# Kernel tuning notes

Hardware: AMD Instinct MI355X
Metric: run time of the kernel (lower is better)

The kernel has to match this reference:

```python
import jax, jax.numpy as jnp
import numpy as np

B_, L_, D_, E_, N_, DT_, K_ = 2, 1024, 1024, 2048, 16, 64, 4
EPS = 1e-5


def setup_inputs() -> dict:
    key = jax.random.key(0)
    ks = jax.random.split(key, 16)
    s = lambda *sh: 1.0 / np.sqrt(sh[-1])
    return {
        "resid": jax.random.normal(ks[0], (B_, L_, D_), jnp.float32),
        "norm_w": jnp.ones((D_,), jnp.float32),
        "skip_w": jax.random.normal(ks[1], (E_, D_), jnp.float32) * s(E_, D_),
        "in_w": jax.random.normal(ks[2], (E_, D_), jnp.float32) * s(E_, D_),
        "conv_w": jax.random.normal(ks[3], (E_, K_), jnp.float32) * s(E_, K_),
        "conv_b": jax.random.normal(ks[4], (E_,), jnp.float32) * 0.1,
        "wd1": jax.random.normal(ks[5], (DT_, E_), jnp.float32) * s(DT_, E_),
        "wd2": jax.random.normal(ks[6], (E_, DT_), jnp.float32) * s(E_, DT_),
        "wd2_b": jax.random.normal(ks[7], (E_,), jnp.float32) * 0.1,
        "wb": jax.random.normal(ks[8], (N_, E_), jnp.float32) * s(N_, E_),
        "wc": jax.random.normal(ks[9], (N_, E_), jnp.float32) * s(N_, E_),
        "A_log": jnp.log(jax.random.uniform(ks[10], (E_, N_), jnp.float32, 0.5, 4.0)),
        "W_D": jnp.ones((E_,), jnp.float32),
        "out_w": jax.random.normal(ks[11], (D_, E_), jnp.float32) * s(D_, E_),
    }


def _forward(resid, norm_w, skip_w, in_w, conv_w, conv_b, wd1, wd2, wd2_b,
             wb, wc, A_log, W_D, out_w):
    B, L, D = resid.shape
    E, N = A_log.shape
    K = conv_w.shape[-1]
    # RMSNorm
    xn = resid * jax.lax.rsqrt(jnp.mean(resid * resid, -1, keepdims=True) + EPS) * norm_w
    skip = jnp.einsum('bld,ed->ble', xn, skip_w)
    x = jnp.einsum('bld,ed->ble', xn, in_w)
    # causal depthwise conv1d (torch pads both sides by K-1, output cut to [:L])
    xp = jnp.pad(x, ((0, 0), (K - 1, 0), (0, 0)))
    conv = conv_b + sum(xp[:, k:k + L, :] * conv_w[:, k] for k in range(K))
    x = jax.nn.silu(conv)  # [B,L,E] ssm input
    # input-dependent projections
    delta = jax.nn.softplus(jnp.einsum('ble,re->blr', x, wd1) @ wd2.T + wd2_b)  # [B,L,E]
    Bt = jnp.einsum('ble,ne->bln', x, wb)  # [B,L,N]
    Ct = jnp.einsum('ble,ne->bln', x, wc)  # [B,L,N]
    A = -jnp.exp(A_log)  # [E,N]

    def step(h, inp):
        dt, b_t, c_t, x_t = inp  # [B,E],[B,N],[B,N],[B,E]
        A_bar = jnp.exp(dt[:, :, None] * A)          # [B,E,N]
        h = A_bar * h + (dt * x_t)[:, :, None] * b_t[:, None, :]
        y = jnp.einsum('ben,bn->be', h, c_t)
        return h, y

    h0 = jnp.zeros((B, E, N), x.dtype)
    xs = (delta.transpose(1, 0, 2), Bt.transpose(1, 0, 2),
          Ct.transpose(1, 0, 2), x.transpose(1, 0, 2))
    _, y = jax.lax.scan(step, h0, xs)
    y = y.transpose(1, 0, 2)  # [B,L,E]
    y = y + x * W_D
    y = y * jax.nn.silu(skip)
    y = jnp.einsum('ble,de->bld', y, out_w)
    return resid + y


def reference(resid, norm_w, skip_w, in_w, conv_w, conv_b, wd1, wd2, wd2_b,
              wb, wc, A_log, W_D, out_w):
    return _forward(resid, norm_w, skip_w, in_w, conv_w, conv_b, wd1, wd2,
                    wd2_b, wb, wc, A_log, W_D, out_w)
```

## Files before the change

kernel.cpp:

```cpp
#include <hip/hip_runtime.h>
#include <cstdint>

typedef unsigned short u16;
typedef float f32x4 __attribute__((ext_vector_type(4)));
typedef __bf16 bf16x8 __attribute__((ext_vector_type(8)));
typedef u16 u16x8 __attribute__((ext_vector_type(8)));

__device__ __forceinline__ u16 f2bf(float f) {
  uint32_t u = __float_as_uint(f);
  u += 0x7fffu + ((u >> 16) & 1u);
  return (u16)(u >> 16);
}
__device__ __forceinline__ float bf2f(u16 s) {
  return __uint_as_float(((uint32_t)s) << 16);
}

__device__ __forceinline__ void ld16(const u16* g, u16* l) {
  auto* gp = reinterpret_cast<const __attribute__((address_space(1))) u16*>(
      reinterpret_cast<uintptr_t>(g));
  auto* lp = reinterpret_cast<__attribute__((address_space(3))) u16*>(
      static_cast<uint32_t>(reinterpret_cast<uintptr_t>(l)));
  __builtin_amdgcn_global_load_lds(gp, lp, 16, 0, 0);
}

__device__ __forceinline__ f32x4 mfma16(u16x8 a, u16x8 b, f32x4 c) {
  return __builtin_amdgcn_mfma_f32_16x16x32_bf16(
      __builtin_bit_cast(bf16x8, a), __builtin_bit_cast(bf16x8, b), c, 0, 0, 0);
}

__device__ __forceinline__ float sigmoidf_(float x) { return 1.f / (1.f + __expf(-x)); }
__device__ __forceinline__ float siluf_(float x) { return x * sigmoidf_(x); }
__device__ __forceinline__ float softplusf_(float x) {
  return fmaxf(x, 0.f) + log1pf(__expf(-fabsf(x)));
}

#define PACK_TOT 6651904
__global__ __launch_bounds__(256) void pack_rms_kernel(
    const float* __restrict__ skip_w, const float* __restrict__ in_w,
    const float* __restrict__ out_w, const float* __restrict__ wd2,
    const float* __restrict__ wd1, const float* __restrict__ wb,
    const float* __restrict__ wc, const float* __restrict__ A_log,
    u16* __restrict__ skipw_bf, u16* __restrict__ inw_bf, u16* __restrict__ outw_bf,
    u16* __restrict__ wd2_bf, u16* __restrict__ w96, float* __restrict__ Aneg,
    const float* __restrict__ resid, const float* __restrict__ norm_w,
    u16* __restrict__ xn_bf) {
  int t = threadIdx.x;
  if (blockIdx.x >= 1024) {
    int row = blockIdx.x - 1024;
    const float4* xr = (const float4*)(resid + (size_t)row * 1024);
    float4 v = xr[t];
    float ss = v.x * v.x + v.y * v.y + v.z * v.z + v.w * v.w;
    for (int o = 32; o > 0; o >>= 1) ss += __shfl_xor(ss, o);
    __shared__ float wsum[4];
    if ((t & 63) == 0) wsum[t >> 6] = ss;
    __syncthreads();
    float tot = wsum[0] + wsum[1] + wsum[2] + wsum[3];
    float rs = rsqrtf(tot * (1.0f / 1024.0f) + 1e-5f);
    float4 wv = ((const float4*)norm_w)[t];
    uint2 pk;
    pk.x = (uint32_t)f2bf(v.x * rs * wv.x) | ((uint32_t)f2bf(v.y * rs * wv.y) << 16);
    pk.y = (uint32_t)f2bf(v.z * rs * wv.z) | ((uint32_t)f2bf(v.w * rs * wv.w) << 16);
    ((uint2*)xn_bf)[row * 256 + t] = pk;
    return;
  }
  const int stride = 1024 * 256;
  for (int i = blockIdx.x * 256 + t; i < PACK_TOT; i += stride) {
    int j = i;
    if (j < 2097152) { skipw_bf[j] = f2bf(skip_w[j]); continue; } j -= 2097152;
    if (j < 2097152) { inw_bf[j] = f2bf(in_w[j]); continue; } j -= 2097152;
    if (j < 2097152) { outw_bf[j] = f2bf(out_w[j]); continue; } j -= 2097152;
    if (j < 131072)  { wd2_bf[j] = f2bf(wd2[j]); continue; } j -= 131072;
    if (j < 131072)  { w96[j] = f2bf(wd1[j]); continue; } j -= 131072;
    if (j < 32768)   { w96[131072 + j] = f2bf(wb[j]); continue; } j -= 32768;
    if (j < 32768)   { w96[163840 + j] = f2bf(wc[j]); continue; } j -= 32768;
    Aneg[j] = -__expf(A_log[j]);
  }
}

template <int BM, int BN, int BK, int EPI>
__global__ __launch_bounds__(256, 4) void gemm_bt(
    const u16* __restrict__ A, const u16* __restrict__ B0, const u16* __restrict__ B1,
    int N, int K, int Kld, int mTiles, int Nsplit,
    void* __restrict__ C0, void* __restrict__ C1) {
  constexpr int TM = BM / 32, TN = BN / 32;
  constexpr int KC = BK / 8;
  __shared__ __align__(16) u16 sA[BM * BK];
  __shared__ __align__(16) u16 sB[BN * BK];
  const int t = threadIdx.x;
  const int lane = t & 63, wid = t >> 6;
  const int wm = wid >> 1, wn = wid & 1;
  const int by = blockIdx.y & (mTiles - 1);
  const int kOff = (blockIdx.y / mTiles) * K;
  const int mBase = by * BM;
  const int nBase = blockIdx.x * BN;
  const bool hi = (nBase >= Nsplit);
  const u16* Bp = hi ? B1 : B0;
  const int nB0 = nBase - (hi ? Nsplit : 0);
  const int col = lane & 15, quad = lane >> 4;

  f32x4 acc[TM][TN];
#pragma unroll
  for (int i = 0; i < TM; ++i)
#pragma unroll
    for (int j = 0; j < TN; ++j) acc[i][j] = f32x4{0.f, 0.f, 0.f, 0.f};

  for (int k0 = kOff; k0 < kOff + K; k0 += BK) {
#pragma unroll
    for (int c = t; c < BM * KC; c += 256) {
      int row = c / KC, j = c % KC;
      int k8 = ((j + row) & (KC - 1)) * 8;
      ld16(A + (size_t)(mBase + row) * Kld + k0 + k8, &sA[c * 8]);
    }
#pragma unroll
    for (int c = t; c < BN * KC; c += 256) {
      int row = c / KC, j = c % KC;
      int k8 = ((j + row) & (KC - 1)) * 8;
      ld16(Bp + (size_t)(nB0 + row) * Kld + k0 + k8, &sB[c * 8]);
    }
    __syncthreads();
#pragma unroll
    for (int kk = 0; kk < BK / 32; ++kk) {
      u16x8 af[TM], bfv[TN];
#pragma unroll
      for (int i = 0; i < TM; ++i) {
        int rowA = wm * (BM / 2) + i * 16 + col;
        af[i] = *(const u16x8*)&sA[rowA * BK + (((kk * 4 + quad) - rowA) & (KC - 1)) * 8];
      }
#pragma unroll
      for (int j = 0; j < TN; ++j) {
        int rowB = wn * (BN / 2) + j * 16 + col;
        bfv[j] = *(const u16x8*)&sB[rowB * BK + (((kk * 4 + quad) - rowB) & (KC - 1)) * 8];
      }
#pragma unroll
      for (int i = 0; i < TM; ++i)
#pragma unroll
        for (int j = 0; j < TN; ++j) acc[i][j] = mfma16(af[i], bfv[j], acc[i][j]);
    }
    __syncthreads();
  }

#pragma unroll
  for (int i = 0; i < TM; ++i) {
#pragma unroll
    for (int j = 0; j < TN; ++j) {
#pragma unroll
      for (int r = 0; r < 4; ++r) {
        int gm = mBase + wm * (BM / 2) + i * 16 + quad * 4 + r;
        int gn = nBase + wn * (BN / 2) + j * 16 + col;
        float v = acc[i][j][r];
        if (EPI == 0) {
          if (gn < Nsplit)
            ((u16*)C0)[(size_t)gm * Nsplit + gn] = f2bf(v);
          else
            ((u16*)C1)[(size_t)gm * (N - Nsplit) + (gn - Nsplit)] = f2bf(v);
        } else {
          atomicAdd(&((float*)C0)[(size_t)gm * N + gn], v);
        }
      }
    }
  }
}

__global__ __launch_bounds__(256) void conv_skinny_kernel(
    const u16* __restrict__ xin_bf, const float* __restrict__ conv_w,
    const float* __restrict__ conv_b, u16* __restrict__ xconv_bf,
    const u16* __restrict__ w96, float* __restrict__ dbc) {
  constexpr int PAD = 136;
  __shared__ __align__(16) u16 sA[64 * PAD];
  __shared__ __align__(16) u16 sB[96 * 128];
  const int t = threadIdx.x, lane = t & 63, w = t >> 6;
  const int mBase = blockIdx.x * 64;
  const int e0 = blockIdx.y * 128;

  {
    const int ep = (t & 63) * 2;
    const int strip = t >> 6;
    const int ms = mBase + strip * 16;
    const int l0 = ms & 1023;
    const uint32_t* xr = (const uint32_t*)xin_bf;
    size_t base = ((size_t)ms * 2048 + e0 + ep) >> 1;
    int eg = e0 + ep;
    float4 w0 = ((const float4*)conv_w)[eg];
    float4 w1 = ((const float4*)conv_w)[eg + 1];
    float b0 = conv_b[eg], b1 = conv_b[eg + 1];
    uint32_t u;
    u = (l0 >= 1) ? xr[base - 1024] : 0u;
    float h10 = bf2f((u16)u), h11 = bf2f((u16)(u >> 16));
    u = (l0 >= 2) ? xr[base - 2048] : 0u;
    float h20 = bf2f((u16)u), h21 = bf2f((u16)(u >> 16));
    u = (l0 >= 3) ? xr[base - 3072] : 0u;
    float h30 = bf2f((u16)u), h31 = bf2f((u16)(u >> 16));
#pragma unroll 4
    for (int r = 0; r < 16; ++r) {
      uint32_t ux = xr[base + (size_t)r * 1024];
      float x0 = bf2f((u16)ux), x1 = bf2f((u16)(ux >> 16));
      float a0 = b0 + w0.w * x0 + w0.z * h10 + w0.y * h20 + w0.x * h30;
      float a1 = b1 + w1.w * x1 + w1.z * h11 + w1.y * h21 + w1.x * h31;
      a0 = siluf_(a0); a1 = siluf_(a1);
      uint32_t pk = (uint32_t)f2bf(a0) | ((uint32_t)f2bf(a1) << 16);
      ((uint32_t*)xconv_bf)[base + (size_t)r * 1024] = pk;
      *(uint32_t*)&sA[(strip * 16 + r) * PAD + ep] = pk;
      h30 = h20; h31 = h21; h20 = h10; h21 = h11; h10 = x0; h11 = x1;
    }
  }
  for (int c = t; c < 96 * 16; c += 256) {
    int row = c >> 4, j = c & 15;
    int k8 = ((j + row) & 15) * 8;
    ld16(w96 + (size_t)row * 2048 + e0 + k8, &sB[c * 8]);
  }
  __syncthreads();
  const int col = lane & 15, quad = lane >> 4;
  const int rowA = w * 16 + col;
  f32x4 acc[6];
#pragma unroll
  for (int j = 0; j < 6; ++j) acc[j] = f32x4{0.f, 0.f, 0.f, 0.f};
#pragma unroll
  for (int kk = 0; kk < 4; ++kk) {
    u16x8 af = *(const u16x8*)&sA[rowA * PAD + kk * 32 + quad * 8];
#pragma unroll
    for (int j = 0; j < 6; ++j) {
      int rowB = j * 16 + col;
      u16x8 bfv = *(const u16x8*)&sB[rowB * 128 + (((kk * 4 + quad) - rowB) & 15) * 8];
      acc[j] = mfma16(af, bfv, acc[j]);
    }
  }
#pragma unroll
  for (int j = 0; j < 6; ++j)
#pragma unroll
    for (int r = 0; r < 4; ++r) {
      int gm = mBase + w * 16 + quad * 4 + r;
      int gn = j * 16 + col;
      atomicAdd(&dbc[gm * 96 + gn], acc[j][r]);
    }
}

__device__ __forceinline__ void delta_tile(
    const float* __restrict__ dbc, const u16* __restrict__ wd2_bf,
    const float* __restrict__ wd2_b, int m0, int e0,
    u16* sD1, float* sDT, float* sBC) {
  const int t = threadIdx.x;
  for (int i = t; i < 2048; i += 256)
    sD1[i] = f2bf(dbc[(m0 + (i >> 6)) * 96 + (i & 63)]);
  for (int j = t; j < 1024; j += 256)
    sBC[j] = dbc[(m0 + (j >> 5)) * 96 + 64 + (j & 31)];
  __syncthreads();
  const int lane = t & 63, wid = t >> 6;
  const int col = lane & 15, quad = lane >> 4;
  const int mt = wid & 1, ntB = (wid >> 1) * 8;
  u16x8 afr0 = *(const u16x8*)&sD1[(mt * 16 + col) * 64 + quad * 8];
  u16x8 afr1 = *(const u16x8*)&sD1[(mt * 16 + col) * 64 + 32 + quad * 8];
#pragma unroll
  for (int jj = 0; jj < 8; ++jj) {
    int ecol = (ntB + jj) * 16 + col;
    int erow = e0 + ecol;
    u16x8 b0 = *(const u16x8*)&wd2_bf[(size_t)erow * 64 + quad * 8];
    u16x8 b1 = *(const u16x8*)&wd2_bf[(size_t)erow * 64 + 32 + quad * 8];
    f32x4 dacc = f32x4{0.f, 0.f, 0.f, 0.f};
    dacc = mfma16(afr0, b0, dacc);
    dacc = mfma16(afr1, b1, dacc);
    float bias = wd2_b[erow];
#pragma unroll
    for (int r = 0; r < 4; ++r)
      sDT[(mt * 16 + quad * 4 + r) * 260 + ecol] = softplusf_(dacc[r] + bias);
  }
  __syncthreads();
}

__global__ __launch_bounds__(256) void scan1_kernel(
    const float* __restrict__ dbc, const u16* __restrict__ wd2_bf,
    const float* __restrict__ wd2_b, const u16* __restrict__ xconv_bf,
    const float* __restrict__ Aneg, float* __restrict__ hloc,
    float* __restrict__ Ssum) {
  __shared__ __align__(16) float sDT[32 * 260];
  __shared__ __align__(16) u16 sD1[32 * 64];
  __shared__ float sBC[1024];
  const int t = threadIdx.x;
  const int eb = blockIdx.x, c = blockIdx.y, b = blockIdx.z;
  const int e0 = eb * 256;
  const int m0 = b * 1024 + c * 32;
  delta_tile(dbc, wd2_bf, wd2_b, m0, e0, sD1, sDT, sBC);
  const int e = e0 + t;
  float Ar[16], h[16];
#pragma unroll
  for (int n = 0; n < 16; ++n) { Ar[n] = Aneg[e * 16 + n]; h[n] = 0.f; }
  float S = 0.f;
  for (int l = 0; l < 32; ++l) {
    size_t m = (size_t)(m0 + l) * 2048 + e;
    float dt = sDT[l * 260 + t];
    float xv = bf2f(xconv_bf[m]);
    S += dt;
    float dx = dt * xv;
    const float* bl = &sBC[l * 32];
#pragma unroll
    for (int n = 0; n < 16; ++n) h[n] = __expf(dt * Ar[n]) * h[n] + dx * bl[n];
  }
  size_t base = ((size_t)(b * 32 + c) * 2048 + e) * 16;
#pragma unroll
  for (int n = 0; n < 16; ++n) hloc[base + n] = h[n];
  Ssum[(b * 32 + c) * 2048 + e] = S;
}

__global__ __launch_bounds__(128) void combine_kernel(
    const float* __restrict__ Aneg, const float* __restrict__ Ssum,
    float* __restrict__ hloc) {
  int tid = blockIdx.x * 128 + threadIdx.x;
  int b = tid >> 15, r = tid & 32767;
  int e = r >> 4;
  float a = Aneg[r];
  float h = 0.f;
  float hl = hloc[(size_t)(b * 32) * 32768 + r];
  float S = Ssum[(b * 32) * 2048 + e];
  for (int c = 0; c < 32; ++c) {
    float hl2 = 0.f, S2 = 0.f;
    if (c < 31) {
      hl2 = hloc[(size_t)(b * 32 + c + 1) * 32768 + r];
      S2 = Ssum[(b * 32 + c + 1) * 2048 + e];
    }
    hloc[(size_t)(b * 32 + c) * 32768 + r] = h;
    h = __expf(a * S) * h + hl;
    hl = hl2; S = S2;
  }
}

__global__ __launch_bounds__(256) void scan2_kernel(
    const float* __restrict__ dbc, const u16* __restrict__ wd2_bf,
    const float* __restrict__ wd2_b, const u16* __restrict__ xconv_bf,
    const float* __restrict__ Aneg, const float* __restrict__ hloc,
    const u16* __restrict__ skip_bf, const float* __restrict__ W_D,
    u16* __restrict__ yfin_bf) {
  __shared__ __align__(16) float sDT[32 * 260];
  __shared__ __align__(16) u16 sD1[32 * 64];
  __shared__ float sBC[1024];
  const int t = threadIdx.x;
  const int eb = blockIdx.x, c = blockIdx.y, b = blockIdx.z;
  const int e0 = eb * 256;
  const int m0 = b * 1024 + c * 32;
  delta_tile(dbc, wd2_bf, wd2_b, m0, e0, sD1, sDT, sBC);
  const int e = e0 + t;
  float Ar[16], h[16];
  size_t hbase = ((size_t)(b * 32 + c) * 2048 + e) * 16;
#pragma unroll
  for (int n = 0; n < 16; ++n) { Ar[n] = Aneg[e * 16 + n]; h[n] = hloc[hbase + n]; }
  float wd = W_D[e];
  for (int l = 0; l < 32; ++l) {
    size_t m = (size_t)(m0 + l) * 2048 + e;
    float dt = sDT[l * 260 + t];
    float xv = bf2f(xconv_bf[m]);
    float dx = dt * xv;
    const float* bl = &sBC[l * 32];
    float y = 0.f;
#pragma unroll
    for (int n = 0; n < 16; ++n) {
      h[n] = __expf(dt * Ar[n]) * h[n] + dx * bl[n];
      y += h[n] * bl[16 + n];
    }
    float yv = y + xv * wd;
    float sk = bf2f(skip_bf[m]);
    yv *= sk * sigmoidf_(sk);
    yfin_bf[m] = f2bf(yv);
  }
}

extern "C" void kernel_launch(void* const* d_in, const int* in_sizes, int n_in,
                              void* d_out, int out_size, void* d_ws, size_t ws_size,
                              hipStream_t stream) {
  (void)in_sizes; (void)n_in; (void)out_size; (void)ws_size;
  const float* resid  = (const float*)d_in[0];
  const float* norm_w = (const float*)d_in[1];
  const float* skip_w = (const float*)d_in[2];
  const float* in_w   = (const float*)d_in[3];
  const float* conv_w = (const float*)d_in[4];
  const float* conv_b = (const float*)d_in[5];
  const float* wd1    = (const float*)d_in[6];
  const float* wd2    = (const float*)d_in[7];
  const float* wd2_b  = (const float*)d_in[8];
  const float* wb     = (const float*)d_in[9];
  const float* wc     = (const float*)d_in[10];
  const float* A_log  = (const float*)d_in[11];
  const float* W_D    = (const float*)d_in[12];
  const float* out_w  = (const float*)d_in[13];

  char* p = (char*)d_ws;
  u16*   skipw_bf = (u16*)(p + 0);
  u16*   inw_bf   = (u16*)(p + 4194304);
  u16*   outw_bf  = (u16*)(p + 8388608);
  u16*   wd2_bf   = (u16*)(p + 12582912);
  u16*   w96      = (u16*)(p + 12845056);
  float* Aneg     = (float*)(p + 13238272);
  u16*   xn_bf    = (u16*)(p + 13369344);
  u16*   skip_bf  = (u16*)(p + 17563648);
  u16*   xin_bf   = (u16*)(p + 25952256);
  u16*   xconv_bf = (u16*)(p + 34340864);
  float* dbc      = (float*)(p + 42729472);
  u16*   yfin_bf  = (u16*)(p + 43515904);
  float* hloc     = (float*)(p + 51904512);
  float* Ssum     = (float*)(p + 60293120);

  hipMemsetAsync((void*)dbc, 0, 2048 * 96 * sizeof(float), stream);
  hipMemcpyAsync(d_out, (const void*)resid, 2048 * 1024 * sizeof(float),
                 hipMemcpyDeviceToDevice, stream);
  pack_rms_kernel<<<3072, 256, 0, stream>>>(
      skip_w, in_w, out_w, wd2, wd1, wb, wc, A_log,
      skipw_bf, inw_bf, outw_bf, wd2_bf, w96, Aneg,
      resid, norm_w, xn_bf);
  gemm_bt<128, 64, 64, 0><<<dim3(64, 16), 256, 0, stream>>>(
      xn_bf, skipw_bf, inw_bf, 4096, 1024, 1024, 16, 2048,
      (void*)skip_bf, (void*)xin_bf);
  conv_skinny_kernel<<<dim3(32, 16), 256, 0, stream>>>(
      xin_bf, conv_w, conv_b, xconv_bf, w96, dbc);
  scan1_kernel<<<dim3(8, 32, 2), 256, 0, stream>>>(
      dbc, wd2_bf, wd2_b, xconv_bf, Aneg, hloc, Ssum);
  combine_kernel<<<512, 128, 0, stream>>>(Aneg, Ssum, hloc);
  scan2_kernel<<<dim3(8, 32, 2), 256, 0, stream>>>(
      dbc, wd2_bf, wd2_b, xconv_bf, Aneg, hloc, skip_bf, W_D, yfin_bf);
  gemm_bt<128, 64, 64, 3><<<dim3(16, 32), 256, 0, stream>>>(
      yfin_bf, outw_bf, outw_bf, 1024, 1024, 2048, 16, 1024,
      (void*)d_out, nullptr);
}
```

Before: 241.4 us.

## Fuse residual copy into pack kernel, stage scan inputs in LDS, prefetch combine loads

The residual-to-output copy moves from a separate device memcpy into extra blocks of the pack/RMSNorm kernel, removing one launch. The scan kernels bulk-load the xconv and skip tiles into LDS with async global-to-LDS loads instead of doing a strided 2-byte global read on every step. The combine kernel preloads all 32 chunk states and sums into registers before the serial recurrence, and its block size doubles. The first GEMM switches to 128x128 tiles and gemm_bt drops its min-blocks launch bound. Together these raise LDS and register use, which may lower occupancy.

```diff
diff --git a/kernel.cpp b/kernel.cpp
--- a/kernel.cpp
+++ b/kernel.cpp
@@ -43,8 +43,16 @@
     u16* __restrict__ skipw_bf, u16* __restrict__ inw_bf, u16* __restrict__ outw_bf,
     u16* __restrict__ wd2_bf, u16* __restrict__ w96, float* __restrict__ Aneg,
     const float* __restrict__ resid, const float* __restrict__ norm_w,
-    u16* __restrict__ xn_bf) {
+    u16* __restrict__ xn_bf, float* __restrict__ outp) {
   int t = threadIdx.x;
+  if (blockIdx.x >= 3072) {
+    int i = (blockIdx.x - 3072) * 256 + t;
+    const float4* src = (const float4*)resid;
+    float4* dst = (float4*)outp;
+    dst[i] = src[i];
+    dst[i + 262144] = src[i + 262144];
+    return;
+  }
   if (blockIdx.x >= 1024) {
     int row = blockIdx.x - 1024;
     const float4* xr = (const float4*)(resid + (size_t)row * 1024);
@@ -78,7 +86,7 @@
 }
 
 template <int BM, int BN, int BK, int EPI>
-__global__ __launch_bounds__(256, 4) void gemm_bt(
+__global__ __launch_bounds__(256) void gemm_bt(
     const u16* __restrict__ A, const u16* __restrict__ B0, const u16* __restrict__ B1,
     int N, int K, int Kld, int mTiles, int Nsplit,
     void* __restrict__ C0, void* __restrict__ C1) {
@@ -266,6 +274,16 @@
   __syncthreads();
 }
 
+__device__ __forceinline__ void stage_tile(const u16* __restrict__ g,
+                                           int m0, int e0, u16* s) {
+  const int t = threadIdx.x;
+#pragma unroll
+  for (int i = t; i < 1024; i += 256) {
+    int row = i >> 5, off = (i & 31) * 8;
+    ld16(g + (size_t)(m0 + row) * 2048 + e0 + off, &s[row * 256 + off]);
+  }
+}
+
 __global__ __launch_bounds__(256) void scan1_kernel(
     const float* __restrict__ dbc, const u16* __restrict__ wd2_bf,
     const float* __restrict__ wd2_b, const u16* __restrict__ xconv_bf,
@@ -274,10 +292,12 @@
   __shared__ __align__(16) float sDT[32 * 260];
   __shared__ __align__(16) u16 sD1[32 * 64];
   __shared__ float sBC[1024];
+  __shared__ __align__(16) u16 sXC[32 * 256];
   const int t = threadIdx.x;
   const int eb = blockIdx.x, c = blockIdx.y, b = blockIdx.z;
   const int e0 = eb * 256;
   const int m0 = b * 1024 + c * 32;
+  stage_tile(xconv_bf, m0, e0, sXC);
   delta_tile(dbc, wd2_bf, wd2_b, m0, e0, sD1, sDT, sBC);
   const int e = e0 + t;
   float Ar[16], h[16];
@@ -285,9 +305,8 @@
   for (int n = 0; n < 16; ++n) { Ar[n] = Aneg[e * 16 + n]; h[n] = 0.f; }
   float S = 0.f;
   for (int l = 0; l < 32; ++l) {
-    size_t m = (size_t)(m0 + l) * 2048 + e;
     float dt = sDT[l * 260 + t];
-    float xv = bf2f(xconv_bf[m]);
+    float xv = bf2f(sXC[l * 256 + t]);
     S += dt;
     float dx = dt * xv;
     const float* bl = &sBC[l * 32];
@@ -300,25 +319,25 @@
   Ssum[(b * 32 + c) * 2048 + e] = S;
 }
 
-__global__ __launch_bounds__(128) void combine_kernel(
+__global__ __launch_bounds__(256) void combine_kernel(
     const float* __restrict__ Aneg, const float* __restrict__ Ssum,
     float* __restrict__ hloc) {
-  int tid = blockIdx.x * 128 + threadIdx.x;
+  int tid = blockIdx.x * 256 + threadIdx.x;
   int b = tid >> 15, r = tid & 32767;
   int e = r >> 4;
   float a = Aneg[r];
+  float hl[32], S[32];
+#pragma unroll
+  for (int c = 0; c < 32; ++c)
+    hl[c] = hloc[(size_t)(b * 32 + c) * 32768 + r];
+#pragma unroll
+  for (int c = 0; c < 32; ++c)
+    S[c] = Ssum[(b * 32 + c) * 2048 + e];
   float h = 0.f;
-  float hl = hloc[(size_t)(b * 32) * 32768 + r];
-  float S = Ssum[(b * 32) * 2048 + e];
+#pragma unroll
   for (int c = 0; c < 32; ++c) {
-    float hl2 = 0.f, S2 = 0.f;
-    if (c < 31) {
-      hl2 = hloc[(size_t)(b * 32 + c + 1) * 32768 + r];
-      S2 = Ssum[(b * 32 + c + 1) * 2048 + e];
-    }
     hloc[(size_t)(b * 32 + c) * 32768 + r] = h;
-    h = __expf(a * S) * h + hl;
-    hl = hl2; S = S2;
+    h = __expf(a * S[c]) * h + hl[c];
   }
 }
 
@@ -331,10 +350,14 @@
   __shared__ __align__(16) float sDT[32 * 260];
   __shared__ __align__(16) u16 sD1[32 * 64];
   __shared__ float sBC[1024];
+  __shared__ __align__(16) u16 sXC[32 * 256];
+  __shared__ __align__(16) u16 sSK[32 * 256];
   const int t = threadIdx.x;
   const int eb = blockIdx.x, c = blockIdx.y, b = blockIdx.z;
   const int e0 = eb * 256;
   const int m0 = b * 1024 + c * 32;
+  stage_tile(xconv_bf, m0, e0, sXC);
+  stage_tile(skip_bf, m0, e0, sSK);
   delta_tile(dbc, wd2_bf, wd2_b, m0, e0, sD1, sDT, sBC);
   const int e = e0 + t;
   float Ar[16], h[16];
@@ -345,7 +368,7 @@
   for (int l = 0; l < 32; ++l) {
     size_t m = (size_t)(m0 + l) * 2048 + e;
     float dt = sDT[l * 260 + t];
-    float xv = bf2f(xconv_bf[m]);
+    float xv = bf2f(sXC[l * 256 + t]);
     float dx = dt * xv;
     const float* bl = &sBC[l * 32];
     float y = 0.f;
@@ -355,7 +378,7 @@
       y += h[n] * bl[16 + n];
     }
     float yv = y + xv * wd;
-    float sk = bf2f(skip_bf[m]);
+    float sk = bf2f(sSK[l * 256 + t]);
     yv *= sk * sigmoidf_(sk);
     yfin_bf[m] = f2bf(yv);
   }
@@ -397,20 +420,18 @@
   float* Ssum     = (float*)(p + 60293120);
 
   hipMemsetAsync((void*)dbc, 0, 2048 * 96 * sizeof(float), stream);
-  hipMemcpyAsync(d_out, (const void*)resid, 2048 * 1024 * sizeof(float),
-                 hipMemcpyDeviceToDevice, stream);
-  pack_rms_kernel<<<3072, 256, 0, stream>>>(
+  pack_rms_kernel<<<4096, 256, 0, stream>>>(
       skip_w, in_w, out_w, wd2, wd1, wb, wc, A_log,
       skipw_bf, inw_bf, outw_bf, wd2_bf, w96, Aneg,
-      resid, norm_w, xn_bf);
-  gemm_bt<128, 64, 64, 0><<<dim3(64, 16), 256, 0, stream>>>(
+      resid, norm_w, xn_bf, (float*)d_out);
+  gemm_bt<128, 128, 64, 0><<<dim3(32, 16), 256, 0, stream>>>(
       xn_bf, skipw_bf, inw_bf, 4096, 1024, 1024, 16, 2048,
       (void*)skip_bf, (void*)xin_bf);
   conv_skinny_kernel<<<dim3(32, 16), 256, 0, stream>>>(
       xin_bf, conv_w, conv_b, xconv_bf, w96, dbc);
   scan1_kernel<<<dim3(8, 32, 2), 256, 0, stream>>>(
       dbc, wd2_bf, wd2_b, xconv_bf, Aneg, hloc, Ssum);
-  combine_kernel<<<512, 128, 0, stream>>>(Aneg, Ssum, hloc);
+  combine_kernel<<<256, 256, 0, stream>>>(Aneg, Ssum, hloc);
   scan2_kernel<<<dim3(8, 32, 2), 256, 0, stream>>>(
       dbc, wd2_bf, wd2_b, xconv_bf, Aneg, hloc, skip_bf, W_D, yfin_bf);
   gemm_bt<128, 64, 64, 3><<<dim3(16, 32), 256, 0, stream>>>(
```

Result: no change. 241.1 us (-0.1%).
